# Performance work log

Measured on AMD Instinct MI355X. Metric: run time of the kernel, lower is better.

Reference implementation:

```python
import jax, jax.numpy as jnp
import numpy as np

VOCAB = 32000
EMBED = 300
HIDDEN = 1150
LAYER_SIZES = [EMBED, HIDDEN, HIDDEN, EMBED]  # in->out per LSTM layer
SCALE = EMBED ** 0.5


def _lstm_layer(x, W_ih, W_hh, b_ih, b_hh):
    """Single-layer batch-first LSTM, zero initial state.
    x: [B,S,D]; W_ih: [4H,D]; W_hh: [4H,H]; biases: [4H].
    PyTorch gate order: i, f, g, o.
    Returns outputs [B,S,H]."""
    B = x.shape[0]
    H = W_hh.shape[1]
    # Precompute input contribution for all timesteps: [S,B,4H]
    x_gates = jnp.einsum('bsd,gd->sbg', x, W_ih) + (b_ih + b_hh)

    def step(carry, xg):
        h, c = carry
        gates = xg + h @ W_hh.T  # [B,4H]
        i, f, g, o = jnp.split(gates, 4, axis=-1)
        i = jax.nn.sigmoid(i)
        f = jax.nn.sigmoid(f)
        g = jnp.tanh(g)
        o = jax.nn.sigmoid(o)
        c = f * c + i * g
        h = o * jnp.tanh(c)
        return (h, c), h

    h0 = jnp.zeros((B, H), dtype=x.dtype)
    c0 = jnp.zeros((B, H), dtype=x.dtype)
    _, hs = jax.lax.scan(step, (h0, c0), x_gates)  # hs: [S,B,H]
    return hs.transpose(1, 0, 2)


def setup_inputs() -> dict:
    key = jax.random.key(0)
    ks = jax.random.split(key, 16)
    inp = {}
    inp['input_ids'] = jax.random.randint(ks[0], (16, 256), 0, VOCAB, dtype=jnp.int32)
    emb = jax.random.uniform(ks[1], (VOCAB, EMBED), dtype=jnp.float32, minval=-0.1, maxval=0.1)
    emb = emb.at[0].set(0.0)  # padding_idx = 0
    inp['embedding'] = emb
    k = 2
    for l in range(3):
        din, dout = LAYER_SIZES[l], LAYER_SIZES[l + 1]
        inp[f'W_ih{l}'] = jax.random.normal(ks[k], (4 * dout, din), dtype=jnp.float32) * (1.0 / np.sqrt(din)); k += 1
        inp[f'W_hh{l}'] = jax.random.normal(ks[k], (4 * dout, dout), dtype=jnp.float32) * (1.0 / np.sqrt(dout)); k += 1
        b_ih = jnp.zeros((4 * dout,), dtype=jnp.float32)
        b_ih = b_ih.at[dout:2 * dout].set(1.0)  # forget-gate bias = 1
        inp[f'b_ih{l}'] = b_ih
        inp[f'b_hh{l}'] = jnp.zeros((4 * dout,), dtype=jnp.float32)
    return inp


def reference(input_ids, embedding,
              W_ih0, W_hh0, b_ih0, b_hh0,
              W_ih1, W_hh1, b_ih1, b_hh1,
              W_ih2, W_hh2, b_ih2, b_hh2):
    # Eval-mode AWD-LSTM forward: all dropouts are identity; scale applied.
    x = embedding[input_ids] * SCALE  # [B,S,E]
    x = _lstm_layer(x, W_ih0, W_hh0, b_ih0, b_hh0)  # [B,S,H]
    x = _lstm_layer(x, W_ih1, W_hh1, b_ih1, b_hh1)  # [B,S,H]
    x = _lstm_layer(x, W_ih2, W_hh2, b_ih2, b_hh2)  # [B,S,E]
    # Tied output projection: Linear(E -> V, bias=False) with weight = embedding
    logits = jnp.einsum('bse,ve->bsv', x, embedding)
    return logits
```

## Files before the change

kernel.cpp:

```cpp
#include <hip/hip_runtime.h>

#define BB 16
#define SS 256
#define NVOCAB 32000
#define NEMB 300

#define CHUNK 6
#define NT 384
#define NSTR 384

typedef float f4_t __attribute__((ext_vector_type(4)));
typedef unsigned int u4_t __attribute__((ext_vector_type(4)));
typedef short bf16x8 __attribute__((ext_vector_type(8)));
typedef float f32x4 __attribute__((ext_vector_type(4)));
typedef unsigned short ushort_t;

__device__ __forceinline__ f4_t load_f4u(const float* p) {
    f4_t v;
    __builtin_memcpy(&v, p, sizeof(f4_t));
    return v;
}

__device__ __forceinline__ void llc_store_u4_drain(u4_t* p, u4_t v) {
    asm volatile("global_store_dwordx4 %0, %1, off sc0 sc1\n\t"
                 "s_waitcnt vmcnt(0)" :: "v"(p), "v"(v) : "memory");
}

__device__ __forceinline__ void llc_load8_wait(
        u4_t& u0, u4_t& u1, u4_t& u2, u4_t& u3,
        u4_t& u4v, u4_t& u5v, u4_t& u6v, u4_t& u7v,
        const u4_t* p0, const u4_t* p1, const u4_t* p2, const u4_t* p3,
        const u4_t* p4, const u4_t* p5, const u4_t* p6, const u4_t* p7) {
    asm volatile(
        "global_load_dwordx4 %0, %8, off sc0 sc1\n\t"
        "global_load_dwordx4 %1, %9, off sc0 sc1\n\t"
        "global_load_dwordx4 %2, %10, off sc0 sc1\n\t"
        "global_load_dwordx4 %3, %11, off sc0 sc1\n\t"
        "global_load_dwordx4 %4, %12, off sc0 sc1\n\t"
        "global_load_dwordx4 %5, %13, off sc0 sc1\n\t"
        "global_load_dwordx4 %6, %14, off sc0 sc1\n\t"
        "global_load_dwordx4 %7, %15, off sc0 sc1\n\t"
        "s_waitcnt vmcnt(0)"
        : "=&v"(u0), "=&v"(u1), "=&v"(u2), "=&v"(u3),
          "=&v"(u4v), "=&v"(u5v), "=&v"(u6v), "=&v"(u7v)
        : "v"(p0), "v"(p1), "v"(p2), "v"(p3),
          "v"(p4), "v"(p5), "v"(p6), "v"(p7)
        : "memory");
}

__global__ void embed_kernel(const int* __restrict__ ids,
                             const float* __restrict__ emb,
                             float* __restrict__ x0) {
    int bs = blockIdx.x;
    int id = ids[bs];
    const float* row = emb + (size_t)id * NEMB;
    float* out = x0 + (size_t)bs * NEMB;
    const float scale = 17.320508075688772f;
    for (int e = threadIdx.x; e < NEMB; e += blockDim.x)
        out[e] = row[e] * scale;
}

__global__ void conv_split(const float* __restrict__ src,
                           ushort_t* __restrict__ hi, ushort_t* __restrict__ lo,
                           int N, int K, int KP, int total) {
    for (int i = blockIdx.x * blockDim.x + threadIdx.x; i < total;
         i += gridDim.x * blockDim.x) {
        int r = i / KP, k = i - r * KP;
        float v = (r < N && k < K) ? src[(size_t)r * K + k] : 0.f;
        unsigned u = __float_as_uint(v);
        unsigned hb = (u + 0x7FFFu + ((u >> 16) & 1u)) >> 16;
        float hf = __uint_as_float(hb << 16);
        float rem = v - hf;
        unsigned u2 = __float_as_uint(rem);
        unsigned lb = (u2 + 0x7FFFu + ((u2 >> 16) & 1u)) >> 16;
        hi[i] = (ushort_t)hb;
        lo[i] = (ushort_t)lb;
    }
}

__global__ __launch_bounds__(256) void gemm_mfma(
        const ushort_t* __restrict__ Ah, const ushort_t* __restrict__ Al,
        const ushort_t* __restrict__ Wh, const ushort_t* __restrict__ Wl,
        float* __restrict__ C, int N, int KP,
        const float* __restrict__ bias_i, const float* __restrict__ bias_h,
        int permuted) {
    constexpr int LD = 40;
    __shared__ ushort_t sA[2][128 * LD];
    __shared__ ushort_t sW[2][128 * LD];
    const int t    = threadIdx.x;
    const int lane = t & 63;
    const int wave = t >> 6;
    const int wm   = wave >> 1, wn = wave & 1;
    const int n0   = blockIdx.x * 128;
    const int m0   = blockIdx.y * 128;

    f32x4 acc[4][4];
    #pragma unroll
    for (int i = 0; i < 4; i++)
        #pragma unroll
        for (int j = 0; j < 4; j++)
            acc[i][j] = (f32x4){0.f, 0.f, 0.f, 0.f};

    const int nkt = KP >> 5;
    for (int kt = 0; kt < nkt; kt++) {
        __syncthreads();
        #pragma unroll
        for (int c = 0; c < 2; c++) {
            int id = t + c * 256;
            int r = id >> 2, kq = id & 3;
            int so = r * LD + kq * 8;
            size_t goA = (size_t)(m0 + r) * KP + kt * 32 + kq * 8;
            size_t goW = (size_t)(n0 + r) * KP + kt * 32 + kq * 8;
            *reinterpret_cast<u4_t*>(&sA[0][so]) = *reinterpret_cast<const u4_t*>(Ah + goA);
            *reinterpret_cast<u4_t*>(&sA[1][so]) = *reinterpret_cast<const u4_t*>(Al + goA);
            *reinterpret_cast<u4_t*>(&sW[0][so]) = *reinterpret_cast<const u4_t*>(Wh + goW);
            *reinterpret_cast<u4_t*>(&sW[1][so]) = *reinterpret_cast<const u4_t*>(Wl + goW);
        }
        __syncthreads();

        bf16x8 ah[4], al[4], wh[4], wl[4];
        #pragma unroll
        for (int i = 0; i < 4; i++) {
            int ro = (wm * 64 + i * 16 + (lane & 15)) * LD + (lane >> 4) * 8;
            int co = (wn * 64 + i * 16 + (lane & 15)) * LD + (lane >> 4) * 8;
            ah[i] = *reinterpret_cast<const bf16x8*>(&sA[0][ro]);
            al[i] = *reinterpret_cast<const bf16x8*>(&sA[1][ro]);
            wh[i] = *reinterpret_cast<const bf16x8*>(&sW[0][co]);
            wl[i] = *reinterpret_cast<const bf16x8*>(&sW[1][co]);
        }
        #pragma unroll
        for (int i = 0; i < 4; i++)
            #pragma unroll
            for (int j = 0; j < 4; j++) {
                acc[i][j] = __builtin_amdgcn_mfma_f32_16x16x32_bf16(ah[i], wh[j], acc[i][j], 0, 0, 0);
                acc[i][j] = __builtin_amdgcn_mfma_f32_16x16x32_bf16(ah[i], wl[j], acc[i][j], 0, 0, 0);
                acc[i][j] = __builtin_amdgcn_mfma_f32_16x16x32_bf16(al[i], wh[j], acc[i][j], 0, 0, 0);
            }
    }

    #pragma unroll
    for (int i = 0; i < 4; i++) {
        int row = m0 + wm * 64 + i * 16 + ((lane >> 4) << 2);
        #pragma unroll
        for (int j = 0; j < 4; j++) {
            int col = n0 + wn * 64 + j * 16 + (lane & 15);
            if (col < N) {
                float bv = bias_i ? (bias_i[col] + bias_h[col]) : 0.f;
                #pragma unroll
                for (int r2 = 0; r2 < 4; r2++) {
                    int m = row + r2;
                    float v = acc[i][j][r2] + bv;
                    size_t idx;
                    if (permuted) {
                        int b_ = m >> 8;
                        int s_ = m & 255;
                        idx = ((size_t)s_ * BB + b_) * (size_t)N + col;
                    } else {
                        idx = (size_t)m * (size_t)N + col;
                    }
                    C[idx] = v;
                }
            }
        }
    }
}

template<int SW, int NCHR>
__global__ __launch_bounds__(NT, 1) void lstm_rec(
        const float* __restrict__ Whh,
        const float* __restrict__ xg,
        float* __restrict__ xout,
        u4_t* __restrict__ hx,
        int H, unsigned TB) {
    constexpr int KP   = 48 * SW;
    constexpr int LDH  = KP + 4;
    constexpr int NSUB = SW / 8;
    constexpr int PRS  = 17;
    constexpr int PSS  = 24 * PRS + 4;
    extern __shared__ __align__(16) float lds[];
    float* ht   = lds;
    float* pbuf = ht + 16 * LDH;
    float* gbuf = pbuf + 24 * PSS;
    float* cbuf = gbuf + NT;
    float* hlx  = cbuf + 96;

    const int t    = threadIdx.x;
    const int lane = t & 63;
    const int wv   = t >> 6;
    const int ks   = t >> 3;
    const int rg   = t & 7;
    const int h0   = blockIdx.x * CHUNK;
    const int G4   = 4 * H;

    const float* wr[3];
    #pragma unroll
    for (int j = 0; j < 3; j++) {
        int r = 3 * rg + j, g = r / CHUNK, l = r - g * CHUNK;
        int grow = ((h0 + l) < H) ? (g * H + h0 + l) : 0;
        wr[j] = Whh + (size_t)grow * (size_t)H;
    }

    for (int i = t; i < 16 * LDH; i += NT) ht[i] = 0.f;
    if (t < 96) cbuf[t] = 0.f;
    __syncthreads();

    const int r_row = t >> 4, r_b = t & 15;
    const int r_g = r_row / CHUNK, r_l = r_row - r_g * CHUNK;
    const int r_h = ((h0 + r_l) < H) ? (h0 + r_l) : h0;
    const float* xgp = xg + (size_t)r_b * G4 + (size_t)r_g * H + r_h;

    const int pairidx = (lane >> 4) & 3;
    const int prow3   = 3 * (lane & 7);

    #pragma unroll 1
    for (int s = 0; s < SS; s++) {
        const u4_t* hcb = hx + (size_t)(s & 1) * (16 * NSTR);
        u4_t*       hpb = hx + (size_t)((s + 1) & 1) * (16 * NSTR);
        const unsigned tgt = TB + (unsigned)s;
        float xgv = xgp[(size_t)s * (size_t)(16 * G4)];

        if (s > 0 && t < NCHR) {
            const u4_t* cb = hcb + t;
            #pragma unroll
            for (int rh = 0; rh < 2; rh++) {
                const u4_t* q0 = cb + (rh * 8 + 0) * NSTR;
                const u4_t* q1 = cb + (rh * 8 + 1) * NSTR;
                const u4_t* q2 = cb + (rh * 8 + 2) * NSTR;
                const u4_t* q3 = cb + (rh * 8 + 3) * NSTR;
                const u4_t* q4 = cb + (rh * 8 + 4) * NSTR;
                const u4_t* q5 = cb + (rh * 8 + 5) * NSTR;
                const u4_t* q6 = cb + (rh * 8 + 6) * NSTR;
                const u4_t* q7 = cb + (rh * 8 + 7) * NSTR;
                u4_t u0, u1, u2, u3, u4v, u5v, u6v, u7v;
                for (;;) {
                    llc_load8_wait(u0, u1, u2, u3, u4v, u5v, u6v, u7v,
                                   q0, q1, q2, q3, q4, q5, q6, q7);
                    int ok = (u0.w >= tgt) & (u1.w >= tgt) & (u2.w >= tgt) & (u3.w >= tgt)
                           & (u4v.w >= tgt) & (u5v.w >= tgt) & (u6v.w >= tgt) & (u7v.w >= tgt);
                    if (ok) break;
                }
                float* d;
                d = ht + (rh * 8 + 0) * LDH + 3 * t;
                d[0] = __uint_as_float(u0.x); d[1] = __uint_as_float(u0.y); d[2] = __uint_as_float(u0.z);
                d = ht + (rh * 8 + 1) * LDH + 3 * t;
                d[0] = __uint_as_float(u1.x); d[1] = __uint_as_float(u1.y); d[2] = __uint_as_float(u1.z);
                d = ht + (rh * 8 + 2) * LDH + 3 * t;
                d[0] = __uint_as_float(u2.x); d[1] = __uint_as_float(u2.y); d[2] = __uint_as_float(u2.z);
                d = ht + (rh * 8 + 3) * LDH + 3 * t;
                d[0] = __uint_as_float(u3.x); d[1] = __uint_as_float(u3.y); d[2] = __uint_as_float(u3.z);
                d = ht + (rh * 8 + 4) * LDH + 3 * t;
                d[0] = __uint_as_float(u4v.x); d[1] = __uint_as_float(u4v.y); d[2] = __uint_as_float(u4v.z);
                d = ht + (rh * 8 + 5) * LDH + 3 * t;
                d[0] = __uint_as_float(u5v.x); d[1] = __uint_as_float(u5v.y); d[2] = __uint_as_float(u5v.z);
                d = ht + (rh * 8 + 6) * LDH + 3 * t;
                d[0] = __uint_as_float(u6v.x); d[1] = __uint_as_float(u6v.y); d[2] = __uint_as_float(u6v.z);
                d = ht + (rh * 8 + 7) * LDH + 3 * t;
                d[0] = __uint_as_float(u7v.x); d[1] = __uint_as_float(u7v.y); d[2] = __uint_as_float(u7v.z);
            }
        }
        __syncthreads();

        float a[3][16];
        #pragma unroll
        for (int j = 0; j < 3; j++)
            #pragma unroll
            for (int b = 0; b < 16; b++) a[j][b] = 0.f;

        if (s > 0) {
            #pragma unroll
            for (int sub = 0; sub < NSUB; sub++) {
                const int kk = ks * SW + sub * 8;
                const int k0 = (kk < H) ? kk : 0;
                const int k1 = (kk + 4 < H) ? (kk + 4) : 0;
                const f4_t w00 = load_f4u(wr[0] + k0), w01 = load_f4u(wr[0] + k1);
                const f4_t w10 = load_f4u(wr[1] + k0), w11 = load_f4u(wr[1] + k1);
                const f4_t w20 = load_f4u(wr[2] + k0), w21 = load_f4u(wr[2] + k1);
                const float* hb = ht + kk;
                #pragma unroll
                for (int b = 0; b < 16; b++) {
                    const f4_t h0v = *reinterpret_cast<const f4_t*>(hb + b * LDH);
                    const f4_t h1v = *reinterpret_cast<const f4_t*>(hb + b * LDH + 4);
                    float acc;
                    acc = a[0][b];
                    acc = fmaf(w00.x, h0v.x, acc); acc = fmaf(w00.y, h0v.y, acc);
                    acc = fmaf(w00.z, h0v.z, acc); acc = fmaf(w00.w, h0v.w, acc);
                    acc = fmaf(w01.x, h1v.x, acc); acc = fmaf(w01.y, h1v.y, acc);
                    acc = fmaf(w01.z, h1v.z, acc); acc = fmaf(w01.w, h1v.w, acc);
                    a[0][b] = acc;
                    acc = a[1][b];
                    acc = fmaf(w10.x, h0v.x, acc); acc = fmaf(w10.y, h0v.y, acc);
                    acc = fmaf(w10.z, h0v.z, acc); acc = fmaf(w10.w, h0v.w, acc);
                    acc = fmaf(w11.x, h1v.x, acc); acc = fmaf(w11.y, h1v.y, acc);
                    acc = fmaf(w11.z, h1v.z, acc); acc = fmaf(w11.w, h1v.w, acc);
                    a[1][b] = acc;
                    acc = a[2][b];
                    acc = fmaf(w20.x, h0v.x, acc); acc = fmaf(w20.y, h0v.y, acc);
                    acc = fmaf(w20.z, h0v.z, acc); acc = fmaf(w20.w, h0v.w, acc);
                    acc = fmaf(w21.x, h1v.x, acc); acc = fmaf(w21.y, h1v.y, acc);
                    acc = fmaf(w21.z, h1v.z, acc); acc = fmaf(w21.w, h1v.w, acc);
                    a[2][b] = acc;
                }
            }
        }

        #pragma unroll
        for (int j = 0; j < 3; j++)
            #pragma unroll
            for (int b = 0; b < 16; b++) {
                float v = a[j][b] + __shfl_xor(a[j][b], 8);
                if ((lane & 8) == 0)
                    pbuf[(wv * 4 + pairidx) * PSS + (prow3 + j) * PRS + b] = v;
            }
        __syncthreads();

        {
            float dot = xgv;
            #pragma unroll
            for (int q = 0; q < 24; q++)
                dot += pbuf[q * PSS + r_row * PRS + r_b];
            gbuf[t] = dot;
        }
        __syncthreads();

        if (t < 96) {
            int l = t >> 4, b = t & 15;
            float gi = gbuf[(0 * CHUNK + l) * 16 + b];
            float gf = gbuf[(1 * CHUNK + l) * 16 + b];
            float gg = gbuf[(2 * CHUNK + l) * 16 + b];
            float go = gbuf[(3 * CHUNK + l) * 16 + b];
            float iv = 1.f / (1.f + expf(-gi));
            float fv = 1.f / (1.f + expf(-gf));
            float gv = tanhf(gg);
            float ov = 1.f / (1.f + expf(-go));
            float c  = fv * cbuf[t] + iv * gv;
            cbuf[t]  = c;
            float hv = ov * tanhf(c);
            hv = ((h0 + l) < H) ? hv : 0.f;
            hlx[b * CHUNK + l] = hv;
            if ((h0 + l) < H)
                xout[(size_t)b * ((size_t)SS * H) + (size_t)s * H + (h0 + l)] = hv;
        }
        __syncthreads();

        if (t < 32) {
            int bq = t >> 1, cj = t & 1;
            u4_t pk;
            pk.x = __float_as_uint(hlx[bq * CHUNK + 3 * cj + 0]);
            pk.y = __float_as_uint(hlx[bq * CHUNK + 3 * cj + 1]);
            pk.z = __float_as_uint(hlx[bq * CHUNK + 3 * cj + 2]);
            pk.w = tgt + 1u;
            llc_store_u4_drain(hpb + bq * NSTR + (h0 / 3 + cj), pk);
        }
    }
}

extern "C" void kernel_launch(void* const* d_in, const int* in_sizes, int n_in,
                              void* d_out, int out_size, void* d_ws, size_t ws_size,
                              hipStream_t stream) {
    const int*   ids  = (const int*)d_in[0];
    const float* emb  = (const float*)d_in[1];
    const float* Wih0 = (const float*)d_in[2];
    const float* Whh0 = (const float*)d_in[3];
    const float* bih0 = (const float*)d_in[4];
    const float* bhh0 = (const float*)d_in[5];
    const float* Wih1 = (const float*)d_in[6];
    const float* Whh1 = (const float*)d_in[7];
    const float* bih1 = (const float*)d_in[8];
    const float* bhh1 = (const float*)d_in[9];
    const float* Wih2 = (const float*)d_in[10];
    const float* Whh2 = (const float*)d_in[11];
    const float* bih2 = (const float*)d_in[12];
    const float* bhh2 = (const float*)d_in[13];
    float* out = (float*)d_out;

    float* ws = (float*)d_ws;
    float* xA = ws;
    float* xB = xA + 1228800;
    float* xg = xB + 4710400;
    u4_t*  hx = (u4_t*)(xg + 18841600);
    (void)in_sizes; (void)n_in; (void)out_size; (void)ws_size;

    ushort_t* sc  = (ushort_t*)d_out;
    ushort_t* tAh = sc;
    ushort_t* tAl = tAh + (size_t)4096 * 1152;
    ushort_t* W0h = tAl + (size_t)4096 * 1152;
    ushort_t* W0l = W0h + (size_t)4608 * 320;
    ushort_t* W1h = W0l + (size_t)4608 * 320;
    ushort_t* W1l = W1h + (size_t)4608 * 1152;
    ushort_t* W2h = W1l + (size_t)4608 * 1152;
    ushort_t* W2l = W2h + (size_t)1280 * 1152;

    ushort_t* fAh = (ushort_t*)xB;
    ushort_t* fAl = fAh + (size_t)4096 * 320;
    ushort_t* fWh = (ushort_t*)xg;
    ushort_t* fWl = fWh + (size_t)32000 * 320;

    hipMemsetAsync(hx, 0, (size_t)2 * 16 * NSTR * 16, stream);

    const size_t lds01 = (size_t)(16 * 1156 + 24 * 412 + NT + 96 + 96) * 4;
    const size_t lds2  = (size_t)(16 * 388  + 24 * 412 + NT + 96 + 96) * 4;

    conv_split<<<dim3(720), dim3(256), 0, stream>>>(Wih0, W0h, W0l, 4600, 300, 320, 4608 * 320);
    conv_split<<<dim3(2048), dim3(256), 0, stream>>>(Wih1, W1h, W1l, 4600, 1150, 1152, 4608 * 1152);
    conv_split<<<dim3(720), dim3(256), 0, stream>>>(Wih2, W2h, W2l, 1200, 1150, 1152, 1280 * 1152);

    embed_kernel<<<dim3(BB * SS), dim3(256), 0, stream>>>(ids, emb, xA);

    conv_split<<<dim3(640), dim3(256), 0, stream>>>(xA, tAh, tAl, 4096, 300, 320, 4096 * 320);
    gemm_mfma<<<dim3(36, 32), dim3(256), 0, stream>>>(tAh, tAl, W0h, W0l, xg,
                                                      4600, 320, bih0, bhh0, 1);
    lstm_rec<24, 384><<<dim3(192), dim3(NT), lds01, stream>>>(Whh0, xg, xB, hx, 1150, 0u);

    conv_split<<<dim3(2048), dim3(256), 0, stream>>>(xB, tAh, tAl, 4096, 1150, 1152, 4096 * 1152);
    gemm_mfma<<<dim3(36, 32), dim3(256), 0, stream>>>(tAh, tAl, W1h, W1l, xg,
                                                      4600, 1152, bih1, bhh1, 1);
    lstm_rec<24, 384><<<dim3(192), dim3(NT), lds01, stream>>>(Whh1, xg, xB, hx, 1150, 256u);

    conv_split<<<dim3(2048), dim3(256), 0, stream>>>(xB, tAh, tAl, 4096, 1150, 1152, 4096 * 1152);
    gemm_mfma<<<dim3(10, 32), dim3(256), 0, stream>>>(tAh, tAl, W2h, W2l, xg,
                                                      1200, 1152, bih2, bhh2, 1);
    lstm_rec<8, 100><<<dim3(50), dim3(NT), lds2, stream>>>(Whh2, xg, xA, hx, 300, 512u);

    conv_split<<<dim3(640), dim3(256), 0, stream>>>(xA, fAh, fAl, 4096, 300, 320, 4096 * 320);
    conv_split<<<dim3(2048), dim3(256), 0, stream>>>(emb, fWh, fWl, 32000, 300, 320, 32000 * 320);

    gemm_mfma<<<dim3(250, 32), dim3(256), 0, stream>>>(fAh, fAl, fWh, fWl, out,
                                                       NVOCAB, 320, nullptr, nullptr, 0);
}
```

Before: 8.438 ms.

## Fuse three LSTM layers into one wavefront-pipelined persistent kernel

Replaces the three sequential recurrent kernels, and the input-projection GEMMs for layers 1 and 2, with a single persistent kernel. Blocks are split by layer: 96 for layer 0, 96 for layer 1, 50 for layer 2. Each downstream layer polls the upstream layer's per-timestep hidden states through flag-tagged LLC buffers and computes its input projection inline in FP32, so all layers run concurrently as a wavefront across timesteps. This removes two full serial 256-step recurrences from the critical path, plus the conv_split and GEMM launches between them. In exchange, each block does more FMA work per step. The layout also relies on all 242 blocks being co-resident on the GPU, since spin-waiting blocks would otherwise deadlock.

```diff
diff --git a/kernel.cpp b/kernel.cpp
--- a/kernel.cpp
+++ b/kernel.cpp
@@ -4,10 +4,7 @@
 #define SS 256
 #define NVOCAB 32000
 #define NEMB 300
-
-#define CHUNK 6
 #define NT 384
-#define NSTR 384
 
 typedef float f4_t __attribute__((ext_vector_type(4)));
 typedef unsigned int u4_t __attribute__((ext_vector_type(4)));
@@ -48,6 +45,97 @@
         : "memory");
 }
 
+__device__ __forceinline__ void stage16rows(const u4_t* base, int rstr, unsigned tgt,
+                                            float* dst, int dstr, int t) {
+    const u4_t* cb = base + t;
+    #pragma unroll
+    for (int rh = 0; rh < 2; rh++) {
+        const u4_t* q0 = cb + (rh * 8 + 0) * rstr;
+        const u4_t* q1 = cb + (rh * 8 + 1) * rstr;
+        const u4_t* q2 = cb + (rh * 8 + 2) * rstr;
+        const u4_t* q3 = cb + (rh * 8 + 3) * rstr;
+        const u4_t* q4 = cb + (rh * 8 + 4) * rstr;
+        const u4_t* q5 = cb + (rh * 8 + 5) * rstr;
+        const u4_t* q6 = cb + (rh * 8 + 6) * rstr;
+        const u4_t* q7 = cb + (rh * 8 + 7) * rstr;
+        u4_t u0, u1, u2, u3, u4v, u5v, u6v, u7v;
+        for (;;) {
+            llc_load8_wait(u0, u1, u2, u3, u4v, u5v, u6v, u7v,
+                           q0, q1, q2, q3, q4, q5, q6, q7);
+            int ok = (u0.w >= tgt) & (u1.w >= tgt) & (u2.w >= tgt) & (u3.w >= tgt)
+                   & (u4v.w >= tgt) & (u5v.w >= tgt) & (u6v.w >= tgt) & (u7v.w >= tgt);
+            if (ok) break;
+        }
+        float* d;
+        d = dst + (rh * 8 + 0) * dstr + 3 * t;
+        d[0] = __uint_as_float(u0.x); d[1] = __uint_as_float(u0.y); d[2] = __uint_as_float(u0.z);
+        d = dst + (rh * 8 + 1) * dstr + 3 * t;
+        d[0] = __uint_as_float(u1.x); d[1] = __uint_as_float(u1.y); d[2] = __uint_as_float(u1.z);
+        d = dst + (rh * 8 + 2) * dstr + 3 * t;
+        d[0] = __uint_as_float(u2.x); d[1] = __uint_as_float(u2.y); d[2] = __uint_as_float(u2.z);
+        d = dst + (rh * 8 + 3) * dstr + 3 * t;
+        d[0] = __uint_as_float(u3.x); d[1] = __uint_as_float(u3.y); d[2] = __uint_as_float(u3.z);
+        d = dst + (rh * 8 + 4) * dstr + 3 * t;
+        d[0] = __uint_as_float(u4v.x); d[1] = __uint_as_float(u4v.y); d[2] = __uint_as_float(u4v.z);
+        d = dst + (rh * 8 + 5) * dstr + 3 * t;
+        d[0] = __uint_as_float(u5v.x); d[1] = __uint_as_float(u5v.y); d[2] = __uint_as_float(u5v.z);
+        d = dst + (rh * 8 + 6) * dstr + 3 * t;
+        d[0] = __uint_as_float(u6v.x); d[1] = __uint_as_float(u6v.y); d[2] = __uint_as_float(u6v.z);
+        d = dst + (rh * 8 + 7) * dstr + 3 * t;
+        d[0] = __uint_as_float(u7v.x); d[1] = __uint_as_float(u7v.y); d[2] = __uint_as_float(u7v.z);
+    }
+}
+
+__device__ __forceinline__ void fma_sub(float (&a)[3][16],
+                                        const float* w0, const float* w1, const float* w2,
+                                        int kk, int klim, const float* hbase, int ldh) {
+    const int k0 = (kk < klim) ? kk : 0;
+    const int k1 = (kk + 4 < klim) ? (kk + 4) : 0;
+    const f4_t w00 = load_f4u(w0 + k0), w01 = load_f4u(w0 + k1);
+    const f4_t w10 = load_f4u(w1 + k0), w11 = load_f4u(w1 + k1);
+    const f4_t w20 = load_f4u(w2 + k0), w21 = load_f4u(w2 + k1);
+    const float* hb = hbase + kk;
+    #pragma unroll
+    for (int b = 0; b < 16; b++) {
+        const f4_t h0v = *reinterpret_cast<const f4_t*>(hb + b * ldh);
+        const f4_t h1v = *reinterpret_cast<const f4_t*>(hb + b * ldh + 4);
+        float acc;
+        acc = a[0][b];
+        acc = fmaf(w00.x, h0v.x, acc); acc = fmaf(w00.y, h0v.y, acc);
+        acc = fmaf(w00.z, h0v.z, acc); acc = fmaf(w00.w, h0v.w, acc);
+        acc = fmaf(w01.x, h1v.x, acc); acc = fmaf(w01.y, h1v.y, acc);
+        acc = fmaf(w01.z, h1v.z, acc); acc = fmaf(w01.w, h1v.w, acc);
+        a[0][b] = acc;
+        acc = a[1][b];
+        acc = fmaf(w10.x, h0v.x, acc); acc = fmaf(w10.y, h0v.y, acc);
+        acc = fmaf(w10.z, h0v.z, acc); acc = fmaf(w10.w, h0v.w, acc);
+        acc = fmaf(w11.x, h1v.x, acc); acc = fmaf(w11.y, h1v.y, acc);
+        acc = fmaf(w11.z, h1v.z, acc); acc = fmaf(w11.w, h1v.w, acc);
+        a[1][b] = acc;
+        acc = a[2][b];
+        acc = fmaf(w20.x, h0v.x, acc); acc = fmaf(w20.y, h0v.y, acc);
+        acc = fmaf(w20.z, h0v.z, acc); acc = fmaf(w20.w, h0v.w, acc);
+        acc = fmaf(w21.x, h1v.x, acc); acc = fmaf(w21.y, h1v.y, acc);
+        acc = fmaf(w21.z, h1v.z, acc); acc = fmaf(w21.w, h1v.w, acc);
+        a[2][b] = acc;
+    }
+}
+
+__device__ __forceinline__ void reduce_wave(float (&a)[3][16], float* pbuf,
+                                            int wv, int lane, int PSS) {
+    #pragma unroll
+    for (int j = 0; j < 3; j++)
+        #pragma unroll
+        for (int b = 0; b < 16; b++) {
+            float v = a[j][b];
+            v += __shfl_xor(v, 8);
+            v += __shfl_xor(v, 16);
+            v += __shfl_xor(v, 32);
+            if (lane < 8)
+                pbuf[wv * PSS + (3 * lane + j) * 17 + b] = v;
+        }
+}
+
 __global__ void embed_kernel(const int* __restrict__ ids,
                              const float* __restrict__ emb,
                              float* __restrict__ x0) {
@@ -165,193 +253,328 @@
     }
 }
 
-template<int SW, int NCHR>
-__global__ __launch_bounds__(NT, 1) void lstm_rec(
-        const float* __restrict__ Whh,
-        const float* __restrict__ xg,
-        float* __restrict__ xout,
-        u4_t* __restrict__ hx,
-        int H, unsigned TB) {
-    constexpr int KP   = 48 * SW;
-    constexpr int LDH  = KP + 4;
-    constexpr int NSUB = SW / 8;
-    constexpr int PRS  = 17;
-    constexpr int PSS  = 24 * PRS + 4;
-    extern __shared__ __align__(16) float lds[];
+
+__device__ void rec_l0(float* lds, int t, int blk,
+                       const float* __restrict__ Whh0,
+                       const float* __restrict__ xg0,
+                       u4_t* __restrict__ h0b) {
     float* ht   = lds;
-    float* pbuf = ht + 16 * LDH;
-    float* gbuf = pbuf + 24 * PSS;
-    float* cbuf = gbuf + NT;
-    float* hlx  = cbuf + 96;
-
-    const int t    = threadIdx.x;
-    const int lane = t & 63;
-    const int wv   = t >> 6;
-    const int ks   = t >> 3;
-    const int rg   = t & 7;
-    const int h0   = blockIdx.x * CHUNK;
-    const int G4   = 4 * H;
-
-    const float* wr[3];
-    #pragma unroll
-    for (int j = 0; j < 3; j++) {
-        int r = 3 * rg + j, g = r / CHUNK, l = r - g * CHUNK;
-        int grow = ((h0 + l) < H) ? (g * H + h0 + l) : 0;
-        wr[j] = Whh + (size_t)grow * (size_t)H;
-    }
-
-    for (int i = t; i < 16 * LDH; i += NT) ht[i] = 0.f;
-    if (t < 96) cbuf[t] = 0.f;
+    float* pbuf = ht + 16 * 1152;
+    float* gbuf = pbuf + 6 * 412;
+    float* cbuf = gbuf + 768;
+    float* hlx  = cbuf + 192;
+    const int lane = t & 63, wv = t >> 6, ks = t >> 3, rg = t & 7;
+    const int h0 = blk * 12;
+
+    const float* wr[2][3];
+    #pragma unroll
+    for (int p = 0; p < 2; p++)
+        #pragma unroll
+        for (int j = 0; j < 3; j++) {
+            int r = 24 * p + 3 * rg + j;
+            int g = r / 12, l = r - g * 12;
+            int lc = ((h0 + l) < 1150) ? l : 0;
+            wr[p][j] = Whh0 + (size_t)(g * 1150 + h0 + lc) * 1150;
+        }
+    const int r0 = t >> 4, b0 = t & 15;
+    const float* xgp[2];
+    #pragma unroll
+    for (int p = 0; p < 2; p++) {
+        int r = 24 * p + r0;
+        int g = r / 12, l = r - g * 12;
+        int lc = ((h0 + l) < 1150) ? l : 0;
+        xgp[p] = xg0 + (size_t)b0 * 4600 + (g * 1150 + h0 + lc);
+    }
+
+    for (int i = t; i < 16 * 1152; i += NT) ht[i] = 0.f;
+    if (t < 192) cbuf[t] = 0.f;
     __syncthreads();
 
-    const int r_row = t >> 4, r_b = t & 15;
-    const int r_g = r_row / CHUNK, r_l = r_row - r_g * CHUNK;
-    const int r_h = ((h0 + r_l) < H) ? (h0 + r_l) : h0;
-    const float* xgp = xg + (size_t)r_b * G4 + (size_t)r_g * H + r_h;
-
-    const int pairidx = (lane >> 4) & 3;
-    const int prow3   = 3 * (lane & 7);
-
-    #pragma unroll 1
     for (int s = 0; s < SS; s++) {
-        const u4_t* hcb = hx + (size_t)(s & 1) * (16 * NSTR);
-        u4_t*       hpb = hx + (size_t)((s + 1) & 1) * (16 * NSTR);
-        const unsigned tgt = TB + (unsigned)s;
-        float xgv = xgp[(size_t)s * (size_t)(16 * G4)];
-
-        if (s > 0 && t < NCHR) {
-            const u4_t* cb = hcb + t;
+        float xgv0 = xgp[0][(size_t)s * 73600];
+        float xgv1 = xgp[1][(size_t)s * 73600];
+        if (s > 0)
+            stage16rows(h0b + (size_t)(s - 1) * 6144, 384, (unsigned)s, ht, 1152, t);
+        __syncthreads();
+
+        #pragma unroll
+        for (int p = 0; p < 2; p++) {
+            float a[3][16];
             #pragma unroll
-            for (int rh = 0; rh < 2; rh++) {
-                const u4_t* q0 = cb + (rh * 8 + 0) * NSTR;
-                const u4_t* q1 = cb + (rh * 8 + 1) * NSTR;
-                const u4_t* q2 = cb + (rh * 8 + 2) * NSTR;
-                const u4_t* q3 = cb + (rh * 8 + 3) * NSTR;
-                const u4_t* q4 = cb + (rh * 8 + 4) * NSTR;
-                const u4_t* q5 = cb + (rh * 8 + 5) * NSTR;
-                const u4_t* q6 = cb + (rh * 8 + 6) * NSTR;
-                const u4_t* q7 = cb + (rh * 8 + 7) * NSTR;
-                u4_t u0, u1, u2, u3, u4v, u5v, u6v, u7v;
-                for (;;) {
-                    llc_load8_wait(u0, u1, u2, u3, u4v, u5v, u6v, u7v,
-                                   q0, q1, q2, q3, q4, q5, q6, q7);
-                    int ok = (u0.w >= tgt) & (u1.w >= tgt) & (u2.w >= tgt) & (u3.w >= tgt)
-                           & (u4v.w >= tgt) & (u5v.w >= tgt) & (u6v.w >= tgt) & (u7v.w >= tgt);
-                    if (ok) break;
-                }
-                float* d;
-                d = ht + (rh * 8 + 0) * LDH + 3 * t;
-                d[0] = __uint_as_float(u0.x); d[1] = __uint_as_float(u0.y); d[2] = __uint_as_float(u0.z);
-                d = ht + (rh * 8 + 1) * LDH + 3 * t;
-                d[0] = __uint_as_float(u1.x); d[1] = __uint_as_float(u1.y); d[2] = __uint_as_float(u1.z);
-                d = ht + (rh * 8 + 2) * LDH + 3 * t;
-                d[0] = __uint_as_float(u2.x); d[1] = __uint_as_float(u2.y); d[2] = __uint_as_float(u2.z);
-                d = ht + (rh * 8 + 3) * LDH + 3 * t;
-                d[0] = __uint_as_float(u3.x); d[1] = __uint_as_float(u3.y); d[2] = __uint_as_float(u3.z);
-                d = ht + (rh * 8 + 4) * LDH + 3 * t;
-                d[0] = __uint_as_float(u4v.x); d[1] = __uint_as_float(u4v.y); d[2] = __uint_as_float(u4v.z);
-                d = ht + (rh * 8 + 5) * LDH + 3 * t;
-                d[0] = __uint_as_float(u5v.x); d[1] = __uint_as_float(u5v.y); d[2] = __uint_as_float(u5v.z);
-                d = ht + (rh * 8 + 6) * LDH + 3 * t;
-                d[0] = __uint_as_float(u6v.x); d[1] = __uint_as_float(u6v.y); d[2] = __uint_as_float(u6v.z);
-                d = ht + (rh * 8 + 7) * LDH + 3 * t;
-                d[0] = __uint_as_float(u7v.x); d[1] = __uint_as_float(u7v.y); d[2] = __uint_as_float(u7v.z);
+            for (int j = 0; j < 3; j++)
+                #pragma unroll
+                for (int b = 0; b < 16; b++) a[j][b] = 0.f;
+            if (s > 0) {
+                #pragma unroll
+                for (int sub = 0; sub < 3; sub++)
+                    fma_sub(a, wr[p][0], wr[p][1], wr[p][2],
+                            ks * 24 + sub * 8, 1150, ht, 1152);
             }
-        }
-        __syncthreads();
-
-        float a[3][16];
-        #pragma unroll
-        for (int j = 0; j < 3; j++)
-            #pragma unroll
-            for (int b = 0; b < 16; b++) a[j][b] = 0.f;
-
-        if (s > 0) {
-            #pragma unroll
-            for (int sub = 0; sub < NSUB; sub++) {
-                const int kk = ks * SW + sub * 8;
-                const int k0 = (kk < H) ? kk : 0;
-                const int k1 = (kk + 4 < H) ? (kk + 4) : 0;
-                const f4_t w00 = load_f4u(wr[0] + k0), w01 = load_f4u(wr[0] + k1);
-                const f4_t w10 = load_f4u(wr[1] + k0), w11 = load_f4u(wr[1] + k1);
-                const f4_t w20 = load_f4u(wr[2] + k0), w21 = load_f4u(wr[2] + k1);
-                const float* hb = ht + kk;
+            reduce_wave(a, pbuf, wv, lane, 412);
+            __syncthreads();
+            {
+                float dot = (p == 0) ? xgv0 : xgv1;
                 #pragma unroll
-                for (int b = 0; b < 16; b++) {
-                    const f4_t h0v = *reinterpret_cast<const f4_t*>(hb + b * LDH);
-                    const f4_t h1v = *reinterpret_cast<const f4_t*>(hb + b * LDH + 4);
-                    float acc;
-                    acc = a[0][b];
-                    acc = fmaf(w00.x, h0v.x, acc); acc = fmaf(w00.y, h0v.y, acc);
-                    acc = fmaf(w00.z, h0v.z, acc); acc = fmaf(w00.w, h0v.w, acc);
-                    acc = fmaf(w01.x, h1v.x, acc); acc = fmaf(w01.y, h1v.y, acc);
-                    acc = fmaf(w01.z, h1v.z, acc); acc = fmaf(w01.w, h1v.w, acc);
-                    a[0][b] = acc;
-                    acc = a[1][b];
-                    acc = fmaf(w10.x, h0v.x, acc); acc = fmaf(w10.y, h0v.y, acc);
-                    acc = fmaf(w10.z, h0v.z, acc); acc = fmaf(w10.w, h0v.w, acc);
-                    acc = fmaf(w11.x, h1v.x, acc); acc = fmaf(w11.y, h1v.y, acc);
-                    acc = fmaf(w11.z, h1v.z, acc); acc = fmaf(w11.w, h1v.w, acc);
-                    a[1][b] = acc;
-                    acc = a[2][b];
-                    acc = fmaf(w20.x, h0v.x, acc); acc = fmaf(w20.y, h0v.y, acc);
-                    acc = fmaf(w20.z, h0v.z, acc); acc = fmaf(w20.w, h0v.w, acc);
-                    acc = fmaf(w21.x, h1v.x, acc); acc = fmaf(w21.y, h1v.y, acc);
-                    acc = fmaf(w21.z, h1v.z, acc); acc = fmaf(w21.w, h1v.w, acc);
-                    a[2][b] = acc;
-                }
+                for (int w = 0; w < 6; w++)
+                    dot += pbuf[w * 412 + r0 * 17 + b0];
+                gbuf[t + p * 384] = dot;
             }
-        }
-
-        #pragma unroll
-        for (int j = 0; j < 3; j++)
-            #pragma unroll
-            for (int b = 0; b < 16; b++) {
-                float v = a[j][b] + __shfl_xor(a[j][b], 8);
-                if ((lane & 8) == 0)
-                    pbuf[(wv * 4 + pairidx) * PSS + (prow3 + j) * PRS + b] = v;
-            }
-        __syncthreads();
-
-        {
-            float dot = xgv;
-            #pragma unroll
-            for (int q = 0; q < 24; q++)
-                dot += pbuf[q * PSS + r_row * PRS + r_b];
-            gbuf[t] = dot;
-        }
-        __syncthreads();
-
-        if (t < 96) {
+            __syncthreads();
+        }
+
+        if (t < 192) {
             int l = t >> 4, b = t & 15;
-            float gi = gbuf[(0 * CHUNK + l) * 16 + b];
-            float gf = gbuf[(1 * CHUNK + l) * 16 + b];
-            float gg = gbuf[(2 * CHUNK + l) * 16 + b];
-            float go = gbuf[(3 * CHUNK + l) * 16 + b];
+            float gi = gbuf[(0 * 12 + l) * 16 + b];
+            float gf = gbuf[(1 * 12 + l) * 16 + b];
+            float gg = gbuf[(2 * 12 + l) * 16 + b];
+            float go = gbuf[(3 * 12 + l) * 16 + b];
             float iv = 1.f / (1.f + expf(-gi));
             float fv = 1.f / (1.f + expf(-gf));
             float gv = tanhf(gg);
             float ov = 1.f / (1.f + expf(-go));
-            float c  = fv * cbuf[t] + iv * gv;
-            cbuf[t]  = c;
+            float c = fv * cbuf[t] + iv * gv;
+            cbuf[t] = c;
             float hv = ov * tanhf(c);
-            hv = ((h0 + l) < H) ? hv : 0.f;
-            hlx[b * CHUNK + l] = hv;
-            if ((h0 + l) < H)
-                xout[(size_t)b * ((size_t)SS * H) + (size_t)s * H + (h0 + l)] = hv;
+            hv = ((h0 + l) < 1150) ? hv : 0.f;
+            hlx[b * 12 + l] = hv;
+        }
+        __syncthreads();
+
+        if (t < 64) {
+            int b = t >> 2, cj = t & 3;
+            u4_t pk;
+            pk.x = __float_as_uint(hlx[b * 12 + 3 * cj + 0]);
+            pk.y = __float_as_uint(hlx[b * 12 + 3 * cj + 1]);
+            pk.z = __float_as_uint(hlx[b * 12 + 3 * cj + 2]);
+            pk.w = (unsigned)(s + 1);
+            llc_store_u4_drain(h0b + (size_t)(s * 16 + b) * 384 + (blk * 4 + cj), pk);
+        }
+    }
+}
+
+__device__ void rec_l1(float* lds, int t, int blk,
+                       const float* __restrict__ Wih1,
+                       const float* __restrict__ Whh1,
+                       const float* __restrict__ bih1,
+                       const float* __restrict__ bhh1,
+                       const u4_t* __restrict__ h0b,
+                       u4_t* __restrict__ h1b) {
+    float* ht0  = lds;
+    float* ht1  = ht0 + 16 * 1152;
+    float* pbuf = ht1 + 16 * 1152;
+    float* gbuf = pbuf + 6 * 412;
+    float* cbuf = gbuf + 768;
+    float* hlx  = cbuf + 192;
+    const int lane = t & 63, wv = t >> 6, ks = t >> 3, rg = t & 7;
+    const int h0 = blk * 12;
+
+    int nrow[2][3];
+    #pragma unroll
+    for (int p = 0; p < 2; p++)
+        #pragma unroll
+        for (int j = 0; j < 3; j++) {
+            int r = 24 * p + 3 * rg + j;
+            int g = r / 12, l = r - g * 12;
+            int lc = ((h0 + l) < 1150) ? l : 0;
+            nrow[p][j] = g * 1150 + h0 + lc;
+        }
+    const int r0 = t >> 4, b0 = t & 15;
+    float bv[2];
+    #pragma unroll
+    for (int p = 0; p < 2; p++) {
+        int r = 24 * p + r0;
+        int g = r / 12, l = r - g * 12;
+        int lc = ((h0 + l) < 1150) ? l : 0;
+        int n = g * 1150 + h0 + lc;
+        bv[p] = bih1[n] + bhh1[n];
+    }
+
+    for (int i = t; i < 2 * 16 * 1152; i += NT) ht0[i] = 0.f;
+    if (t < 192) cbuf[t] = 0.f;
+    __syncthreads();
+
+    for (int s = 0; s < SS; s++) {
+        stage16rows(h0b + (size_t)s * 6144, 384, (unsigned)(s + 1), ht0, 1152, t);
+        if (s > 0)
+            stage16rows(h1b + (size_t)(s - 1) * 6144, 384, (unsigned)s, ht1, 1152, t);
+        __syncthreads();
+
+        #pragma unroll
+        for (int p = 0; p < 2; p++) {
+            float a[3][16];
+            #pragma unroll
+            for (int j = 0; j < 3; j++)
+                #pragma unroll
+                for (int b = 0; b < 16; b++) a[j][b] = 0.f;
+            const float* wi0 = Wih1 + (size_t)nrow[p][0] * 1150;
+            const float* wi1 = Wih1 + (size_t)nrow[p][1] * 1150;
+            const float* wi2 = Wih1 + (size_t)nrow[p][2] * 1150;
+            #pragma unroll
+            for (int sub = 0; sub < 3; sub++)
+                fma_sub(a, wi0, wi1, wi2, ks * 24 + sub * 8, 1150, ht0, 1152);
+            if (s > 0) {
+                const float* wh0 = Whh1 + (size_t)nrow[p][0] * 1150;
+                const float* wh1 = Whh1 + (size_t)nrow[p][1] * 1150;
+                const float* wh2 = Whh1 + (size_t)nrow[p][2] * 1150;
+                #pragma unroll
+                for (int sub = 0; sub < 3; sub++)
+                    fma_sub(a, wh0, wh1, wh2, ks * 24 + sub * 8, 1150, ht1, 1152);
+            }
+            reduce_wave(a, pbuf, wv, lane, 412);
+            __syncthreads();
+            {
+                float dot = bv[p];
+                #pragma unroll
+                for (int w = 0; w < 6; w++)
+                    dot += pbuf[w * 412 + r0 * 17 + b0];
+                gbuf[t + p * 384] = dot;
+            }
+            __syncthreads();
+        }
+
+        if (t < 192) {
+            int l = t >> 4, b = t & 15;
+            float gi = gbuf[(0 * 12 + l) * 16 + b];
+            float gf = gbuf[(1 * 12 + l) * 16 + b];
+            float gg = gbuf[(2 * 12 + l) * 16 + b];
+            float go = gbuf[(3 * 12 + l) * 16 + b];
+            float iv = 1.f / (1.f + expf(-gi));
+            float fv = 1.f / (1.f + expf(-gf));
+            float gv = tanhf(gg);
+            float ov = 1.f / (1.f + expf(-go));
+            float c = fv * cbuf[t] + iv * gv;
+            cbuf[t] = c;
+            float hv = ov * tanhf(c);
+            hv = ((h0 + l) < 1150) ? hv : 0.f;
+            hlx[b * 12 + l] = hv;
+        }
+        __syncthreads();
+
+        if (t < 64) {
+            int b = t >> 2, cj = t & 3;
+            u4_t pk;
+            pk.x = __float_as_uint(hlx[b * 12 + 3 * cj + 0]);
+            pk.y = __float_as_uint(hlx[b * 12 + 3 * cj + 1]);
+            pk.z = __float_as_uint(hlx[b * 12 + 3 * cj + 2]);
+            pk.w = (unsigned)(s + 1);
+            llc_store_u4_drain(h1b + (size_t)(s * 16 + b) * 384 + (blk * 4 + cj), pk);
+        }
+    }
+}
+
+__device__ void rec_l2(float* lds, int t, int blk,
+                       const float* __restrict__ Wih2,
+                       const float* __restrict__ Whh2,
+                       const float* __restrict__ bih2,
+                       const float* __restrict__ bhh2,
+                       const u4_t* __restrict__ h1b,
+                       u4_t* __restrict__ h2b,
+                       float* __restrict__ xout) {
+    float* ht1  = lds;
+    float* ht2  = ht1 + 16 * 1152;
+    float* pbuf = ht2 + 16 * 384;
+    float* gbuf = pbuf + 6 * 412;
+    float* cbuf = gbuf + 384;
+    float* hlx  = cbuf + 96;
+    const int lane = t & 63, wv = t >> 6, ks = t >> 3, rg = t & 7;
+    const int h0c = blk * 6;
+
+    const float* wi[3];
+    const float* wh[3];
+    #pragma unroll
+    for (int j = 0; j < 3; j++) {
+        int r = 3 * rg + j;
+        int g = r / 6, l = r - g * 6;
+        int n = g * 300 + h0c + l;
+        wi[j] = Wih2 + (size_t)n * 1150;
+        wh[j] = Whh2 + (size_t)n * 300;
+    }
+    const int r0 = t >> 4, b0 = t & 15;
+    float bv;
+    {
+        int g = r0 / 6, l = r0 - g * 6;
+        int n = g * 300 + h0c + l;
+        bv = bih2[n] + bhh2[n];
+    }
+
+    for (int i = t; i < 16 * 1152 + 16 * 384; i += NT) ht1[i] = 0.f;
+    if (t < 96) cbuf[t] = 0.f;
+    __syncthreads();
+
+    for (int s = 0; s < SS; s++) {
+        stage16rows(h1b + (size_t)s * 6144, 384, (unsigned)(s + 1), ht1, 1152, t);
+        if (s > 0 && t < 100)
+            stage16rows(h2b + (size_t)(s - 1) * 2048, 128, (unsigned)s, ht2, 384, t);
+        __syncthreads();
+
+        float a[3][16];
+        #pragma unroll
+        for (int j = 0; j < 3; j++)
+            #pragma unroll
+            for (int b = 0; b < 16; b++) a[j][b] = 0.f;
+        #pragma unroll
+        for (int sub = 0; sub < 3; sub++)
+            fma_sub(a, wi[0], wi[1], wi[2], ks * 24 + sub * 8, 1150, ht1, 1152);
+        if (s > 0)
+            fma_sub(a, wh[0], wh[1], wh[2], ks * 8, 300, ht2, 384);
+        reduce_wave(a, pbuf, wv, lane, 412);
+        __syncthreads();
+        {
+            float dot = bv;
+            #pragma unroll
+            for (int w = 0; w < 6; w++)
+                dot += pbuf[w * 412 + r0 * 17 + b0];
+            gbuf[t] = dot;
+        }
+        __syncthreads();
+
+        if (t < 96) {
+            int l = t >> 4, b = t & 15;
+            float gi = gbuf[(0 * 6 + l) * 16 + b];
+            float gf = gbuf[(1 * 6 + l) * 16 + b];
+            float gg = gbuf[(2 * 6 + l) * 16 + b];
+            float go = gbuf[(3 * 6 + l) * 16 + b];
+            float iv = 1.f / (1.f + expf(-gi));
+            float fv = 1.f / (1.f + expf(-gf));
+            float gv = tanhf(gg);
+            float ov = 1.f / (1.f + expf(-go));
+            float c = fv * cbuf[t] + iv * gv;
+            cbuf[t] = c;
+            float hv = ov * tanhf(c);
+            hlx[b * 6 + l] = hv;
+            xout[(size_t)(b * 256 + s) * 300 + h0c + l] = hv;
         }
         __syncthreads();
 
         if (t < 32) {
-            int bq = t >> 1, cj = t & 1;
+            int b = t >> 1, cj = t & 1;
             u4_t pk;
-            pk.x = __float_as_uint(hlx[bq * CHUNK + 3 * cj + 0]);
-            pk.y = __float_as_uint(hlx[bq * CHUNK + 3 * cj + 1]);
-            pk.z = __float_as_uint(hlx[bq * CHUNK + 3 * cj + 2]);
-            pk.w = tgt + 1u;
-            llc_store_u4_drain(hpb + bq * NSTR + (h0 / 3 + cj), pk);
-        }
-    }
+            pk.x = __float_as_uint(hlx[b * 6 + 3 * cj + 0]);
+            pk.y = __float_as_uint(hlx[b * 6 + 3 * cj + 1]);
+            pk.z = __float_as_uint(hlx[b * 6 + 3 * cj + 2]);
+            pk.w = (unsigned)(s + 1);
+            llc_store_u4_drain(h2b + (size_t)(s * 16 + b) * 128 + (blk * 2 + cj), pk);
+        }
+    }
+}
+
+__global__ __launch_bounds__(NT, 1) void lstm_fused(
+        const float* __restrict__ Whh0, const float* __restrict__ xg0,
+        const float* __restrict__ Wih1, const float* __restrict__ Whh1,
+        const float* __restrict__ bih1, const float* __restrict__ bhh1,
+        const float* __restrict__ Wih2, const float* __restrict__ Whh2,
+        const float* __restrict__ bih2, const float* __restrict__ bhh2,
+        u4_t* __restrict__ h0b, u4_t* __restrict__ h1b, u4_t* __restrict__ h2b,
+        float* __restrict__ xout) {
+    extern __shared__ __align__(16) float lds[];
+    const int t = threadIdx.x;
+    const int blk = blockIdx.x;
+    if (blk < 96)
+        rec_l0(lds, t, blk, Whh0, xg0, h0b);
+    else if (blk < 192)
+        rec_l1(lds, t, blk - 96, Wih1, Whh1, bih1, bhh1, h0b, h1b);
+    else
+        rec_l2(lds, t, blk - 192, Wih2, Whh2, bih2, bhh2, h1b, h2b, xout);
 }
 
 extern "C" void kernel_launch(void* const* d_in, const int* in_sizes, int n_in,
@@ -372,58 +595,42 @@
     const float* bih2 = (const float*)d_in[12];
     const float* bhh2 = (const float*)d_in[13];
     float* out = (float*)d_out;
-
-    float* ws = (float*)d_ws;
-    float* xA = ws;
-    float* xB = xA + 1228800;
-    float* xg = xB + 4710400;
-    u4_t*  hx = (u4_t*)(xg + 18841600);
     (void)in_sizes; (void)n_in; (void)out_size; (void)ws_size;
+
+    float* ws  = (float*)d_ws;
+    float* xA  = ws;
+    float* xB  = xA + 1228800;
+    float* xg0 = xB + 4710400;
 
     ushort_t* sc  = (ushort_t*)d_out;
     ushort_t* tAh = sc;
-    ushort_t* tAl = tAh + (size_t)4096 * 1152;
-    ushort_t* W0h = tAl + (size_t)4096 * 1152;
+    ushort_t* tAl = tAh + (size_t)4096 * 320;
+    ushort_t* W0h = tAl + (size_t)4096 * 320;
     ushort_t* W0l = W0h + (size_t)4608 * 320;
-    ushort_t* W1h = W0l + (size_t)4608 * 320;
-    ushort_t* W1l = W1h + (size_t)4608 * 1152;
-    ushort_t* W2h = W1l + (size_t)4608 * 1152;
-    ushort_t* W2l = W2h + (size_t)1280 * 1152;
+    u4_t* h0b = (u4_t*)((char*)d_out + ((size_t)16 << 20));
+    u4_t* h1b = h0b + (size_t)256 * 16 * 384;
+    u4_t* h2b = h1b + (size_t)256 * 16 * 384;
 
     ushort_t* fAh = (ushort_t*)xB;
     ushort_t* fAl = fAh + (size_t)4096 * 320;
-    ushort_t* fWh = (ushort_t*)xg;
+    ushort_t* fWh = (ushort_t*)xg0;
     ushort_t* fWl = fWh + (size_t)32000 * 320;
 
-    hipMemsetAsync(hx, 0, (size_t)2 * 16 * NSTR * 16, stream);
-
-    const size_t lds01 = (size_t)(16 * 1156 + 24 * 412 + NT + 96 + 96) * 4;
-    const size_t lds2  = (size_t)(16 * 388  + 24 * 412 + NT + 96 + 96) * 4;
+    hipMemsetAsync(h0b, 0, ((size_t)256 * 16 * (384 + 384 + 128)) * 16, stream);
 
     conv_split<<<dim3(720), dim3(256), 0, stream>>>(Wih0, W0h, W0l, 4600, 300, 320, 4608 * 320);
-    conv_split<<<dim3(2048), dim3(256), 0, stream>>>(Wih1, W1h, W1l, 4600, 1150, 1152, 4608 * 1152);
-    conv_split<<<dim3(720), dim3(256), 0, stream>>>(Wih2, W2h, W2l, 1200, 1150, 1152, 1280 * 1152);
-
     embed_kernel<<<dim3(BB * SS), dim3(256), 0, stream>>>(ids, emb, xA);
-
     conv_split<<<dim3(640), dim3(256), 0, stream>>>(xA, tAh, tAl, 4096, 300, 320, 4096 * 320);
-    gemm_mfma<<<dim3(36, 32), dim3(256), 0, stream>>>(tAh, tAl, W0h, W0l, xg,
+    gemm_mfma<<<dim3(36, 32), dim3(256), 0, stream>>>(tAh, tAl, W0h, W0l, xg0,
                                                       4600, 320, bih0, bhh0, 1);
-    lstm_rec<24, 384><<<dim3(192), dim3(NT), lds01, stream>>>(Whh0, xg, xB, hx, 1150, 0u);
-
-    conv_split<<<dim3(2048), dim3(256), 0, stream>>>(xB, tAh, tAl, 4096, 1150, 1152, 4096 * 1152);
-    gemm_mfma<<<dim3(36, 32), dim3(256), 0, stream>>>(tAh, tAl, W1h, W1l, xg,
-                                                      4600, 1152, bih1, bhh1, 1);
-    lstm_rec<24, 384><<<dim3(192), dim3(NT), lds01, stream>>>(Whh1, xg, xB, hx, 1150, 256u);
-
-    conv_split<<<dim3(2048), dim3(256), 0, stream>>>(xB, tAh, tAl, 4096, 1150, 1152, 4096 * 1152);
-    gemm_mfma<<<dim3(10, 32), dim3(256), 0, stream>>>(tAh, tAl, W2h, W2l, xg,
-                                                      1200, 1152, bih2, bhh2, 1);
-    lstm_rec<8, 100><<<dim3(50), dim3(NT), lds2, stream>>>(Whh2, xg, xA, hx, 300, 512u);
+
+    const size_t ldsF = (size_t)(2 * 16 * 1152 + 6 * 412 + 768 + 192 + 192) * 4;
+    lstm_fused<<<dim3(242), dim3(NT), ldsF, stream>>>(
+        Whh0, xg0, Wih1, Whh1, bih1, bhh1, Wih2, Whh2, bih2, bhh2,
+        h0b, h1b, h2b, xA);
 
     conv_split<<<dim3(640), dim3(256), 0, stream>>>(xA, fAh, fAl, 4096, 300, 320, 4096 * 320);
     conv_split<<<dim3(2048), dim3(256), 0, stream>>>(emb, fWh, fWl, 32000, 300, 320, 32000 * 320);
-
     gemm_mfma<<<dim3(250, 32), dim3(256), 0, stream>>>(fAh, fAl, fWh, fWl, out,
                                                        NVOCAB, 320, nullptr, nullptr, 0);
 }
```

After: 12.30 ms. 45.8% more time.
